# Kernel tuning notes

Measured on AMD Instinct MI355X. Metric: run time of the kernel, lower is better.

## Reference

```python
import jax, jax.numpy as jnp
import numpy as np

N_NODES = 100000
D = 128            # node feature dim == hidden_units[0]
N_EDGES = 640000
BN_EPS = 1e-3      # keras BatchNormalization default epsilon


def setup_inputs() -> dict:
    key = jax.random.key(0)
    ks = jax.random.split(key, 12)
    node_repr = jax.random.normal(ks[0], (N_NODES, D), dtype=jnp.float32)
    edges = jax.random.randint(ks[1], (2, N_EDGES), 0, N_NODES, dtype=jnp.int64)
    # ffn_prepare: BN(D) -> Dense(D, gelu)   (dropout inactive at inference)
    bn1_gamma = jax.random.normal(ks[2], (D,), dtype=jnp.float32) * 0.1 + 1.0
    bn1_beta = jax.random.normal(ks[3], (D,), dtype=jnp.float32) * 0.1
    bn1_mean = jax.random.normal(ks[4], (D,), dtype=jnp.float32) * 0.1
    bn1_var = jax.random.uniform(ks[5], (D,), dtype=jnp.float32) + 0.5
    W1 = jax.random.normal(ks[6], (D, D), dtype=jnp.float32) / np.sqrt(D)
    b1 = jnp.zeros((D,), dtype=jnp.float32)
    # update_fn: BN(2D) -> Dense(D, gelu)
    bn2_gamma = jax.random.normal(ks[7], (2 * D,), dtype=jnp.float32) * 0.1 + 1.0
    bn2_beta = jax.random.normal(ks[8], (2 * D,), dtype=jnp.float32) * 0.1
    bn2_mean = jax.random.normal(ks[9], (2 * D,), dtype=jnp.float32) * 0.1
    bn2_var = jax.random.uniform(ks[10], (2 * D,), dtype=jnp.float32) + 0.5
    W2 = jax.random.normal(ks[11], (2 * D, D), dtype=jnp.float32) / np.sqrt(2 * D)
    b2 = jnp.zeros((D,), dtype=jnp.float32)
    return dict(node_repr=node_repr, edges=edges,
                bn1_gamma=bn1_gamma, bn1_beta=bn1_beta, bn1_mean=bn1_mean, bn1_var=bn1_var,
                W1=W1, b1=b1,
                bn2_gamma=bn2_gamma, bn2_beta=bn2_beta, bn2_mean=bn2_mean, bn2_var=bn2_var,
                W2=W2, b2=b2)


def _bn(x, gamma, beta, mean, var):
    # inference-mode batch norm
    return (x - mean) * jax.lax.rsqrt(var + BN_EPS) * gamma + beta


def reference(node_repr, edges, bn1_gamma, bn1_beta, bn1_mean, bn1_var, W1, b1,
              bn2_gamma, bn2_beta, bn2_mean, bn2_var, W2, b2):
    num_nodes = node_repr.shape[0]
    node_indices, neighbour_indices = edges[0], edges[1]
    # gather neighbour features: [E, D]
    neigh = node_repr[neighbour_indices]
    # prepare FFN (BN -> dropout(identity at eval) -> Dense + exact gelu)
    msg = jax.nn.gelu(_bn(neigh, bn1_gamma, bn1_beta, bn1_mean, bn1_var) @ W1 + b1,
                      approximate=False)
    # unsorted_segment_mean: sum / count, empty segments -> 0 (TF semantics)
    sums = jax.ops.segment_sum(msg, node_indices, num_segments=num_nodes)
    cnt = jax.ops.segment_sum(jnp.ones((edges.shape[1],), msg.dtype), node_indices,
                              num_segments=num_nodes)
    agg = sums / jnp.maximum(cnt, 1.0)[:, None]
    # update FFN on concat [node_repr, agg]: [N, 2D] -> [N, D]
    h = jnp.concatenate([node_repr, agg], axis=1)
    out = jax.nn.gelu(_bn(h, bn2_gamma, bn2_beta, bn2_mean, bn2_var) @ W2 + b2,
                      approximate=False)
    return out
```

## Files before the change

kernel.cpp:

```cpp
#include <hip/hip_runtime.h>

#define NN 100000
#define DD 128
#define EE 640000
#define BN_EPS 1e-3f
#define NBLK 391
#define NTILE 6250
#define EPB 1637
#define FFN2_BLKS 768

typedef __bf16 bf16x8 __attribute__((ext_vector_type(8)));
typedef float f32x4 __attribute__((ext_vector_type(4)));

#define W1F_OFF 0u
#define W2F_OFF 32768u
#define B1F_OFF 98304u
#define B2F_OFF 98816u
#define T_OFF   99328u
#define OFFS_OFF 26099328u
#define ELIST_OFF 26899328u
#define CNTG_OFF ELIST_OFF
#define BOFS_OFF (ELIST_OFF + 611524u)
#define BSUM_OFF 29459328u
#define BOFF_OFF 29461376u
#define AGG_OFF 29464576u
#define XB_OFF  55064576u

__device__ __forceinline__ float gelu_fast(float x) {
    float x3 = x * x * x;
    float z2 = 1.5957691216057308f * x + 0.07135481627002407f * x3;
    return x / (1.0f + __expf(-z2));
}

__global__ __launch_bounds__(256) void prep_kernel(
    const float* __restrict__ g1, const float* __restrict__ be1,
    const float* __restrict__ m1, const float* __restrict__ v1,
    const float* __restrict__ W1, const float* __restrict__ b1,
    const float* __restrict__ g2, const float* __restrict__ be2,
    const float* __restrict__ m2, const float* __restrict__ v2,
    const float* __restrict__ W2, const float* __restrict__ b2,
    const int* __restrict__ edges,
    __bf16* __restrict__ W1f, __bf16* __restrict__ W2f,
    float* __restrict__ b1f, float* __restrict__ b2f,
    int* __restrict__ cntg)
{
    const int blk = blockIdx.x;
    const int t = threadIdx.x;
    if (blk < 64) {
        const int w = (blk * 256 + t) >> 6;
        const int lane = t & 63;
        if (w < 128) {
            float acc = 0.f;
            for (int k = lane; k < 128; k += 64) {
                float s = g1[k] * rsqrtf(v1[k] + BN_EPS);
                float sh = be1[k] - m1[k] * s;
                acc += sh * W1[k * 128 + w];
            }
#pragma unroll
            for (int off = 32; off > 0; off >>= 1) acc += __shfl_down(acc, off);
            if (lane == 0) b1f[w] = acc + b1[w];
        } else {
            const int n = w - 128;
            float acc = 0.f;
            for (int k = lane; k < 256; k += 64) {
                float s = g2[k] * rsqrtf(v2[k] + BN_EPS);
                float sh = be2[k] - m2[k] * s;
                acc += sh * W2[k * 128 + n];
            }
#pragma unroll
            for (int off = 32; off > 0; off >>= 1) acc += __shfl_down(acc, off);
            if (lane == 0) b2f[n] = acc + b2[n];
        }
    } else if (blk < 256) {
        int tid = (blk - 64) * 256 + t;
        if (tid < 16384) {
            int idx = tid;
            int i = idx & 7, l = (idx >> 3) & 63, nt = (idx >> 9) & 7, kt = idx >> 12;
            int k = kt * 32 + (l >> 4) * 8 + i;
            int n = nt * 16 + (l & 15);
            float s = g1[k] * rsqrtf(v1[k] + BN_EPS);
            W1f[idx] = (__bf16)(s * W1[k * 128 + n]);
        } else {
            int idx = tid - 16384;
            int i = idx & 7, l = (idx >> 3) & 63, nt = (idx >> 9) & 7, kt = idx >> 12;
            int n = nt * 16 + (l & 15);
            int row;
            if (kt < 4) {
                row = kt * 32 + (l >> 4) * 8 + i;
            } else {
                int q = (kt - 4) * 32 + (l >> 4) * 8 + i;
                row = 128 + ((q & 7) * 16 + (q >> 3));
            }
            float s = g2[row] * rsqrtf(v2[row] + BN_EPS);
            W2f[idx] = (__bf16)(s * W2[row * 128 + n]);
        }
    } else {
        __shared__ int cnt[NBLK];
        const int k = blk - 256;
        for (int b = t; b < NBLK; b += 256) cnt[b] = 0;
        __syncthreads();
        const int e0 = k * EPB, e1 = min(e0 + EPB, EE);
        for (int e = e0 + t; e < e1; e += 256)
            atomicAdd(&cnt[edges[e] >> 8], 1);
        __syncthreads();
        for (int b = t; b < NBLK; b += 256) cntg[k * NBLK + b] = cnt[b];
    }
}

__global__ __launch_bounds__(256) void sortb_kernel(const int* __restrict__ cntg,
                                                    int* __restrict__ bofs,
                                                    int* __restrict__ bsum)
{
    const int b = blockIdx.x, t = threadIdx.x;
    __shared__ int sp[256];
    int ia = 2 * t, ib = 2 * t + 1;
    int va = (ia < NBLK) ? cntg[ia * NBLK + b] : 0;
    int vb = (ib < NBLK) ? cntg[ib * NBLK + b] : 0;
    sp[t] = va + vb;
    __syncthreads();
    for (int off = 1; off < 256; off <<= 1) {
        int tmp = (t >= off) ? sp[t - off] : 0;
        __syncthreads();
        sp[t] += tmp;
        __syncthreads();
    }
    int pexcl = sp[t] - (va + vb);
    if (ia < NBLK) bofs[b * NBLK + ia] = pexcl;
    if (ib < NBLK) bofs[b * NBLK + ib] = pexcl + va;
    if (t == 255) bsum[b] = sp[255];
}

__global__ __launch_bounds__(512) void scan_top_kernel(const int* __restrict__ bsum,
                                                       int* __restrict__ boff)
{
    __shared__ int s[512];
    const int t = threadIdx.x;
    int v = (t < NBLK) ? bsum[t] : 0;
    s[t] = v;
    __syncthreads();
    for (int off = 1; off < 512; off <<= 1) {
        int tmp = (t >= off) ? s[t - off] : 0;
        __syncthreads();
        s[t] += tmp;
        __syncthreads();
    }
    if (t < NBLK) boff[t] = s[t] - v;
}

__global__ __launch_bounds__(256) void sortc_ffn1_kernel(
    const int* __restrict__ edges, const int* __restrict__ boff,
    const int* __restrict__ bofs, int* __restrict__ pairbuf,
    const float* __restrict__ X, const __bf16* __restrict__ W1f,
    const float* __restrict__ b1f, __bf16* __restrict__ T,
    __bf16* __restrict__ Xb)
{
    __shared__ __bf16 sW[16384];
    const int t = threadIdx.x;
    if (blockIdx.x < NBLK) {
        int* cur = (int*)sW;
        const int k = blockIdx.x;
        for (int b = t; b < NBLK; b += 256)
            cur[b] = boff[b] + bofs[b * NBLK + k];
        __syncthreads();
        const int e0 = k * EPB, e1 = min(e0 + EPB, EE);
        for (int e = e0 + t; e < e1; e += 256) {
            int dst = edges[e];
            int src = edges[EE + e];
            int pos = atomicAdd(&cur[dst >> 8], 1);
            pairbuf[pos] = (src << 8) | (dst & 255);
        }
        return;
    }
#pragma unroll
    for (int i = 0; i < 8; ++i) {
        int ch = i * 256 + t;
        *(bf16x8*)(sW + ch * 8) = *(const bf16x8*)(W1f + (size_t)ch * 8);
    }
    __syncthreads();

    const int wave = t >> 6;
    const int lane = t & 63;
    const int c = lane & 15, kh = lane >> 4;
    const int tbase = (blockIdx.x - NBLK) * 8;

    float bias[8];
#pragma unroll
    for (int nt = 0; nt < 8; ++nt) bias[nt] = b1f[nt * 16 + c];

#pragma unroll
    for (int s = 0; s < 2; ++s) {
        const int tile = tbase + s * 4 + wave;
        if (tile >= NTILE) break;
        const size_t rowb = (size_t)(tile * 16 + c) * DD;
        const float* xr = X + rowb + kh * 8;
        f32x4 r0[4], r1[4];
#pragma unroll
        for (int q = 0; q < 4; ++q) {
            r0[q] = *(const f32x4*)(xr + q * 32);
            r1[q] = *(const f32x4*)(xr + q * 32 + 4);
        }
        bf16x8 af[4];
#pragma unroll
        for (int kt = 0; kt < 4; ++kt) {
            bf16x8 fa;
#pragma unroll
            for (int i = 0; i < 4; ++i) { fa[i] = (__bf16)r0[kt][i]; fa[4 + i] = (__bf16)r1[kt][i]; }
            af[kt] = fa;
        }
#pragma unroll
        for (int kt = 0; kt < 4; ++kt)
            *(bf16x8*)(Xb + rowb + kt * 32 + kh * 8) = af[kt];

        f32x4 acc[8] = {};
#pragma unroll
        for (int kt = 0; kt < 4; ++kt)
#pragma unroll
            for (int nt = 0; nt < 8; ++nt) {
                bf16x8 bfr = *(const bf16x8*)(sW + ((kt * 8 + nt) * 64 + lane) * 8);
                acc[nt] = __builtin_amdgcn_mfma_f32_16x16x32_bf16(af[kt], bfr, acc[nt], 0, 0, 0);
            }
#pragma unroll
        for (int r = 0; r < 4; ++r) {
            int row = tile * 16 + kh * 4 + r;
            bf16x8 o;
#pragma unroll
            for (int nt = 0; nt < 8; ++nt)
                o[nt] = (__bf16)gelu_fast(acc[nt][r] + bias[nt]);
            *(bf16x8*)(T + (size_t)row * DD + c * 8) = o;
        }
    }
}

__global__ __launch_bounds__(256) void p2_kernel(const int* __restrict__ boff,
                                                 const int* __restrict__ pairbuf,
                                                 int* __restrict__ elist,
                                                 int* __restrict__ offs)
{
    __shared__ int s[256];
    __shared__ int cur[256];
    const int b = blockIdx.x, t = threadIdx.x;
    const int start = boff[b];
    const int end = (b + 1 < NBLK) ? boff[b + 1] : EE;
    cur[t] = 0;
    __syncthreads();
    for (int e = start + t; e < end; e += 256)
        atomicAdd(&cur[pairbuf[e] & 255], 1);
    __syncthreads();
    int v = cur[t];
    s[t] = v;
    __syncthreads();
    for (int off = 1; off < 256; off <<= 1) {
        int tmp = (t >= off) ? s[t - off] : 0;
        __syncthreads();
        s[t] += tmp;
        __syncthreads();
    }
    int ex = s[t] - v + start;
    const int node = b * 256 + t;
    if (node <= NN) offs[node] = ex;
    __syncthreads();
    cur[t] = ex;
    __syncthreads();
    for (int e = start + t; e < end; e += 256) {
        int item = pairbuf[e];
        int pos = atomicAdd(&cur[item & 255], 1);
        elist[pos] = item >> 8;
    }
}

__global__ __launch_bounds__(256) void agg_kernel(
    const __bf16* __restrict__ T, const int* __restrict__ offs,
    const int* __restrict__ elist, __bf16* __restrict__ Agg)
{
    int t = blockIdx.x * 256 + threadIdx.x;
    int node = t >> 4, j = t & 15;
    if (node >= NN) return;
    const int lane = threadIdx.x & 63;
    const int gbase = lane & 48;
    const int beg = offs[node];
    const int end = offs[node + 1];
    const int d = end - beg;
    float acc[8] = {};
    for (int eb = beg; eb < end; eb += 16) {
        int me = eb + (lane & 15);
        int sv = (me < end) ? elist[me] : 0;
        int cnt = min(end - eb, 16);
        int i = 0;
        for (; i + 3 < cnt; i += 4) {
            int s0 = __shfl(sv, gbase + i);
            int s1 = __shfl(sv, gbase + i + 1);
            int s2 = __shfl(sv, gbase + i + 2);
            int s3 = __shfl(sv, gbase + i + 3);
            bf16x8 v0 = *(const bf16x8*)(T + (size_t)s0 * DD + j * 8);
            bf16x8 v1 = *(const bf16x8*)(T + (size_t)s1 * DD + j * 8);
            bf16x8 v2 = *(const bf16x8*)(T + (size_t)s2 * DD + j * 8);
            bf16x8 v3 = *(const bf16x8*)(T + (size_t)s3 * DD + j * 8);
#pragma unroll
            for (int q = 0; q < 8; ++q)
                acc[q] += ((float)v0[q] + (float)v1[q]) + ((float)v2[q] + (float)v3[q]);
        }
        for (; i < cnt; ++i) {
            int s0 = __shfl(sv, gbase + i);
            bf16x8 v0 = *(const bf16x8*)(T + (size_t)s0 * DD + j * 8);
#pragma unroll
            for (int q = 0; q < 8; ++q) acc[q] += (float)v0[q];
        }
    }
    const float inv = 1.0f / fmaxf((float)d, 1.0f);
    bf16x8 o;
#pragma unroll
    for (int q = 0; q < 8; ++q) o[q] = (__bf16)(acc[q] * inv);
    *(bf16x8*)(Agg + (size_t)node * DD + j * 8) = o;
}

#define FFN2_LOAD(TT, XA, GA)                                              \
    {                                                                      \
        const size_t rb = (size_t)((TT) * 16 + c) * DD + kh * 8;           \
        _Pragma("unroll")                                                  \
        for (int q = 0; q < 4; ++q) {                                      \
            XA[q] = *(const bf16x8*)(Xb + rb + q * 32);                    \
            GA[q] = *(const bf16x8*)(Agg + rb + q * 32);                   \
        }                                                                  \
    }

#define FFN2_COMP(TT, XA, GA)                                              \
    {                                                                      \
        f32x4 acc0 = {}, acc1 = {};                                        \
        _Pragma("unroll")                                                  \
        for (int kt = 0; kt < 4; ++kt) {                                   \
            acc0 = __builtin_amdgcn_mfma_f32_16x16x32_bf16(XA[kt], Bf[kt][0], acc0, 0, 0, 0); \
            acc1 = __builtin_amdgcn_mfma_f32_16x16x32_bf16(XA[kt], Bf[kt][1], acc1, 0, 0, 0); \
        }                                                                  \
        _Pragma("unroll")                                                  \
        for (int kt = 0; kt < 4; ++kt) {                                   \
            acc0 = __builtin_amdgcn_mfma_f32_16x16x32_bf16(GA[kt], Bf[4 + kt][0], acc0, 0, 0, 0); \
            acc1 = __builtin_amdgcn_mfma_f32_16x16x32_bf16(GA[kt], Bf[4 + kt][1], acc1, 0, 0, 0); \
        }                                                                  \
        _Pragma("unroll")                                                  \
        for (int r = 0; r < 4; ++r) {                                      \
            int row = (TT) * 16 + kh * 4 + r;                              \
            out[(size_t)row * DD + (w * 2) * 16 + c] = gelu_fast(acc0[r] + bias0); \
            out[(size_t)row * DD + (w * 2 + 1) * 16 + c] = gelu_fast(acc1[r] + bias1); \
        }                                                                  \
    }

__global__ __launch_bounds__(256) void ffn2_kernel(
    const __bf16* __restrict__ Xb, const __bf16* __restrict__ Agg,
    const __bf16* __restrict__ W2f, const float* __restrict__ b2f,
    float* __restrict__ out)
{
    const int w = threadIdx.x >> 6;
    const int lane = threadIdx.x & 63;
    const int c = lane & 15, kh = lane >> 4;
    const int G = gridDim.x;

    bf16x8 Bf[8][2];
#pragma unroll
    for (int kt = 0; kt < 8; ++kt) {
        Bf[kt][0] = *(const bf16x8*)(W2f + ((size_t)((kt * 8 + w * 2) * 64 + lane)) * 8);
        Bf[kt][1] = *(const bf16x8*)(W2f + ((size_t)((kt * 8 + w * 2 + 1) * 64 + lane)) * 8);
    }
    const float bias0 = b2f[(w * 2) * 16 + c];
    const float bias1 = b2f[(w * 2 + 1) * 16 + c];

    int tile = blockIdx.x;
    if (tile >= NTILE) return;
    bf16x8 xa[4], ga[4], xb2[4], gb[4];
    FFN2_LOAD(tile, xa, ga);
    while (true) {
        int t2 = tile + G;
        if (t2 < NTILE) FFN2_LOAD(t2, xb2, gb);
        FFN2_COMP(tile, xa, ga);
        if (t2 >= NTILE) break;
        int t3 = t2 + G;
        if (t3 < NTILE) FFN2_LOAD(t3, xa, ga);
        FFN2_COMP(t2, xb2, gb);
        if (t3 >= NTILE) break;
        tile = t3;
    }
}

extern "C" void kernel_launch(void* const* d_in, const int* in_sizes, int n_in,
                              void* d_out, int out_size, void* d_ws, size_t ws_size,
                              hipStream_t stream) {
    const float* node_repr = (const float*)d_in[0];
    const int*   edges     = (const int*)d_in[1];
    const float* g1 = (const float*)d_in[2];
    const float* be1 = (const float*)d_in[3];
    const float* m1 = (const float*)d_in[4];
    const float* v1 = (const float*)d_in[5];
    const float* W1 = (const float*)d_in[6];
    const float* b1 = (const float*)d_in[7];
    const float* g2 = (const float*)d_in[8];
    const float* be2 = (const float*)d_in[9];
    const float* m2 = (const float*)d_in[10];
    const float* v2 = (const float*)d_in[11];
    const float* W2 = (const float*)d_in[12];
    const float* b2 = (const float*)d_in[13];

    char* ws = (char*)d_ws;
    __bf16* W1f = (__bf16*)(ws + W1F_OFF);
    __bf16* W2f = (__bf16*)(ws + W2F_OFF);
    float* b1f = (float*)(ws + B1F_OFF);
    float* b2f = (float*)(ws + B2F_OFF);
    __bf16* T  = (__bf16*)(ws + T_OFF);
    int* offs  = (int*)(ws + OFFS_OFF);
    int* elist = (int*)(ws + ELIST_OFF);
    int* cntg  = (int*)(ws + CNTG_OFF);
    int* bofs  = (int*)(ws + BOFS_OFF);
    int* bsum  = (int*)(ws + BSUM_OFF);
    int* boff  = (int*)(ws + BOFF_OFF);
    __bf16* Agg = (__bf16*)(ws + AGG_OFF);
    int* pairbuf = (int*)(ws + AGG_OFF);
    __bf16* Xb = (__bf16*)(ws + XB_OFF);
    float* out = (float*)d_out;

    hipLaunchKernelGGL(prep_kernel, dim3(256 + NBLK), dim3(256), 0, stream,
                       g1, be1, m1, v1, W1, b1, g2, be2, m2, v2, W2, b2,
                       edges, W1f, W2f, b1f, b2f, cntg);

    hipLaunchKernelGGL(sortb_kernel, dim3(NBLK), dim3(256), 0, stream, cntg, bofs, bsum);
    hipLaunchKernelGGL(scan_top_kernel, dim3(1), dim3(512), 0, stream, bsum, boff);

    hipLaunchKernelGGL(sortc_ffn1_kernel, dim3(NBLK + (NTILE + 7) / 8), dim3(256), 0, stream,
                       edges, boff, bofs, pairbuf, node_repr, W1f, b1f, T, Xb);

    hipLaunchKernelGGL(p2_kernel, dim3(NBLK), dim3(256), 0, stream,
                       boff, pairbuf, elist, offs);

    hipLaunchKernelGGL(agg_kernel, dim3((NN * 16 + 255) / 256), dim3(256), 0, stream,
                       T, offs, elist, Agg);

    hipLaunchKernelGGL(ffn2_kernel, dim3(FFN2_BLKS), dim3(256), 0, stream,
                       Xb, Agg, W2f, b2f, out);
}
```

Measured before the change: 106.7 us.

## Fold top-level scan into sort kernels and co-schedule FFN1 with bucket pass

Removes the single-block scan_top kernel. Each sortc block now recomputes the bucket prefix from bsum itself, and each p2 block computes its start offset with a wave-shuffle reduction. FFN1 tiles move out of the scatter kernel and share a launch with the per-bucket counting-sort pass, and the two tiles per wave have their global loads issued before either is computed. This cuts one launch and its serialization at the cost of redundant prefix work in every block.

```diff
diff --git a/kernel.cpp b/kernel.cpp
--- a/kernel.cpp
+++ b/kernel.cpp
@@ -7,6 +7,7 @@
 #define NBLK 391
 #define NTILE 6250
 #define EPB 1637
+#define FFN1_BLKS 782
 #define FFN2_BLKS 768
 
 typedef __bf16 bf16x8 __attribute__((ext_vector_type(8)));
@@ -22,7 +23,6 @@
 #define CNTG_OFF ELIST_OFF
 #define BOFS_OFF (ELIST_OFF + 611524u)
 #define BSUM_OFF 29459328u
-#define BOFF_OFF 29461376u
 #define AGG_OFF 29464576u
 #define XB_OFF  55064576u
 
@@ -130,26 +130,41 @@
     if (t == 255) bsum[b] = sp[255];
 }
 
-__global__ __launch_bounds__(512) void scan_top_kernel(const int* __restrict__ bsum,
-                                                       int* __restrict__ boff)
-{
-    __shared__ int s[512];
-    const int t = threadIdx.x;
-    int v = (t < NBLK) ? bsum[t] : 0;
-    s[t] = v;
+__global__ __launch_bounds__(256) void sortc_kernel(const int* __restrict__ edges,
+                                                    const int* __restrict__ bsum,
+                                                    const int* __restrict__ bofs,
+                                                    int* __restrict__ pairbuf)
+{
+    __shared__ int sp[256];
+    __shared__ int cur[NBLK];
+    const int k = blockIdx.x, t = threadIdx.x;
+    int ia = 2 * t, ib = 2 * t + 1;
+    int va = (ia < NBLK) ? bsum[ia] : 0;
+    int vb = (ib < NBLK) ? bsum[ib] : 0;
+    sp[t] = va + vb;
     __syncthreads();
-    for (int off = 1; off < 512; off <<= 1) {
-        int tmp = (t >= off) ? s[t - off] : 0;
-        __syncthreads();
-        s[t] += tmp;
-        __syncthreads();
-    }
-    if (t < NBLK) boff[t] = s[t] - v;
-}
-
-__global__ __launch_bounds__(256) void sortc_ffn1_kernel(
-    const int* __restrict__ edges, const int* __restrict__ boff,
-    const int* __restrict__ bofs, int* __restrict__ pairbuf,
+    for (int off = 1; off < 256; off <<= 1) {
+        int tmp = (t >= off) ? sp[t - off] : 0;
+        __syncthreads();
+        sp[t] += tmp;
+        __syncthreads();
+    }
+    int pexcl = sp[t] - (va + vb);
+    if (ia < NBLK) cur[ia] = pexcl + bofs[ia * NBLK + k];
+    if (ib < NBLK) cur[ib] = pexcl + va + bofs[ib * NBLK + k];
+    __syncthreads();
+    const int e0 = k * EPB, e1 = min(e0 + EPB, EE);
+    for (int e = e0 + t; e < e1; e += 256) {
+        int dst = edges[e];
+        int src = edges[EE + e];
+        int pos = atomicAdd(&cur[dst >> 8], 1);
+        pairbuf[pos] = (src << 8) | (dst & 255);
+    }
+}
+
+__global__ __launch_bounds__(256) void p2_ffn1_kernel(
+    const int* __restrict__ bsum, const int* __restrict__ pairbuf,
+    int* __restrict__ elist, int* __restrict__ offs,
     const float* __restrict__ X, const __bf16* __restrict__ W1f,
     const float* __restrict__ b1f, __bf16* __restrict__ T,
     __bf16* __restrict__ Xb)
@@ -157,17 +172,41 @@
     __shared__ __bf16 sW[16384];
     const int t = threadIdx.x;
     if (blockIdx.x < NBLK) {
-        int* cur = (int*)sW;
-        const int k = blockIdx.x;
-        for (int b = t; b < NBLK; b += 256)
-            cur[b] = boff[b] + bofs[b * NBLK + k];
-        __syncthreads();
-        const int e0 = k * EPB, e1 = min(e0 + EPB, EE);
-        for (int e = e0 + t; e < e1; e += 256) {
-            int dst = edges[e];
-            int src = edges[EE + e];
-            int pos = atomicAdd(&cur[dst >> 8], 1);
-            pairbuf[pos] = (src << 8) | (dst & 255);
+        int* sArr = (int*)sW;
+        int* cur  = sArr + 256;
+        int* red  = sArr + 512;
+        const int b = blockIdx.x;
+        int part = 0;
+        for (int i = t; i < b; i += 256) part += bsum[i];
+#pragma unroll
+        for (int off = 32; off > 0; off >>= 1) part += __shfl_down(part, off);
+        if ((t & 63) == 0) red[t >> 6] = part;
+        cur[t] = 0;
+        __syncthreads();
+        const int start = red[0] + red[1] + red[2] + red[3];
+        const int end = start + bsum[b];
+        for (int e = start + t; e < end; e += 256)
+            atomicAdd(&cur[pairbuf[e] & 255], 1);
+        __syncthreads();
+        int v = cur[t];
+        sArr[t] = v;
+        __syncthreads();
+        for (int off = 1; off < 256; off <<= 1) {
+            int tmp = (t >= off) ? sArr[t - off] : 0;
+            __syncthreads();
+            sArr[t] += tmp;
+            __syncthreads();
+        }
+        int ex = sArr[t] - v + start;
+        const int node = b * 256 + t;
+        if (node <= NN) offs[node] = ex;
+        __syncthreads();
+        cur[t] = ex;
+        __syncthreads();
+        for (int e = start + t; e < end; e += 256) {
+            int item = pairbuf[e];
+            int pos = atomicAdd(&cur[item & 255], 1);
+            elist[pos] = item >> 8;
         }
         return;
     }
@@ -182,35 +221,43 @@
     const int lane = t & 63;
     const int c = lane & 15, kh = lane >> 4;
     const int tbase = (blockIdx.x - NBLK) * 8;
+    const int tile0 = tbase + wave;
+    const int tile1 = tbase + 4 + wave;
 
     float bias[8];
 #pragma unroll
     for (int nt = 0; nt < 8; ++nt) bias[nt] = b1f[nt * 16 + c];
 
-#pragma unroll
-    for (int s = 0; s < 2; ++s) {
-        const int tile = tbase + s * 4 + wave;
-        if (tile >= NTILE) break;
-        const size_t rowb = (size_t)(tile * 16 + c) * DD;
-        const float* xr = X + rowb + kh * 8;
-        f32x4 r0[4], r1[4];
+    f32x4 r0[4], r1[4], s0[4], s1[4];
+    bf16x8 af[4];
+
+    if (tile0 < NTILE) {
+        const float* xr = X + (size_t)(tile0 * 16 + c) * DD + kh * 8;
 #pragma unroll
         for (int q = 0; q < 4; ++q) {
             r0[q] = *(const f32x4*)(xr + q * 32);
             r1[q] = *(const f32x4*)(xr + q * 32 + 4);
         }
-        bf16x8 af[4];
+    }
+    if (tile1 < NTILE) {
+        const float* xr = X + (size_t)(tile1 * 16 + c) * DD + kh * 8;
+#pragma unroll
+        for (int q = 0; q < 4; ++q) {
+            s0[q] = *(const f32x4*)(xr + q * 32);
+            s1[q] = *(const f32x4*)(xr + q * 32 + 4);
+        }
+    }
+
+    if (tile0 < NTILE) {
+        const size_t rowb = (size_t)(tile0 * 16 + c) * DD;
 #pragma unroll
         for (int kt = 0; kt < 4; ++kt) {
             bf16x8 fa;
 #pragma unroll
             for (int i = 0; i < 4; ++i) { fa[i] = (__bf16)r0[kt][i]; fa[4 + i] = (__bf16)r1[kt][i]; }
             af[kt] = fa;
-        }
-#pragma unroll
-        for (int kt = 0; kt < 4; ++kt)
-            *(bf16x8*)(Xb + rowb + kt * 32 + kh * 8) = af[kt];
-
+            *(bf16x8*)(Xb + rowb + kt * 32 + kh * 8) = fa;
+        }
         f32x4 acc[8] = {};
 #pragma unroll
         for (int kt = 0; kt < 4; ++kt)
@@ -221,7 +268,7 @@
             }
 #pragma unroll
         for (int r = 0; r < 4; ++r) {
-            int row = tile * 16 + kh * 4 + r;
+            int row = tile0 * 16 + kh * 4 + r;
             bf16x8 o;
 #pragma unroll
             for (int nt = 0; nt < 8; ++nt)
@@ -229,42 +276,33 @@
             *(bf16x8*)(T + (size_t)row * DD + c * 8) = o;
         }
     }
-}
-
-__global__ __launch_bounds__(256) void p2_kernel(const int* __restrict__ boff,
-                                                 const int* __restrict__ pairbuf,
-                                                 int* __restrict__ elist,
-                                                 int* __restrict__ offs)
-{
-    __shared__ int s[256];
-    __shared__ int cur[256];
-    const int b = blockIdx.x, t = threadIdx.x;
-    const int start = boff[b];
-    const int end = (b + 1 < NBLK) ? boff[b + 1] : EE;
-    cur[t] = 0;
-    __syncthreads();
-    for (int e = start + t; e < end; e += 256)
-        atomicAdd(&cur[pairbuf[e] & 255], 1);
-    __syncthreads();
-    int v = cur[t];
-    s[t] = v;
-    __syncthreads();
-    for (int off = 1; off < 256; off <<= 1) {
-        int tmp = (t >= off) ? s[t - off] : 0;
-        __syncthreads();
-        s[t] += tmp;
-        __syncthreads();
-    }
-    int ex = s[t] - v + start;
-    const int node = b * 256 + t;
-    if (node <= NN) offs[node] = ex;
-    __syncthreads();
-    cur[t] = ex;
-    __syncthreads();
-    for (int e = start + t; e < end; e += 256) {
-        int item = pairbuf[e];
-        int pos = atomicAdd(&cur[item & 255], 1);
-        elist[pos] = item >> 8;
+    if (tile1 < NTILE) {
+        const size_t rowb = (size_t)(tile1 * 16 + c) * DD;
+#pragma unroll
+        for (int kt = 0; kt < 4; ++kt) {
+            bf16x8 fa;
+#pragma unroll
+            for (int i = 0; i < 4; ++i) { fa[i] = (__bf16)s0[kt][i]; fa[4 + i] = (__bf16)s1[kt][i]; }
+            af[kt] = fa;
+            *(bf16x8*)(Xb + rowb + kt * 32 + kh * 8) = fa;
+        }
+        f32x4 acc[8] = {};
+#pragma unroll
+        for (int kt = 0; kt < 4; ++kt)
+#pragma unroll
+            for (int nt = 0; nt < 8; ++nt) {
+                bf16x8 bfr = *(const bf16x8*)(sW + ((kt * 8 + nt) * 64 + lane) * 8);
+                acc[nt] = __builtin_amdgcn_mfma_f32_16x16x32_bf16(af[kt], bfr, acc[nt], 0, 0, 0);
+            }
+#pragma unroll
+        for (int r = 0; r < 4; ++r) {
+            int row = tile1 * 16 + kh * 4 + r;
+            bf16x8 o;
+#pragma unroll
+            for (int nt = 0; nt < 8; ++nt)
+                o[nt] = (__bf16)gelu_fast(acc[nt][r] + bias[nt]);
+            *(bf16x8*)(T + (size_t)row * DD + c * 8) = o;
+        }
     }
 }
 
@@ -409,7 +447,6 @@
     int* cntg  = (int*)(ws + CNTG_OFF);
     int* bofs  = (int*)(ws + BOFS_OFF);
     int* bsum  = (int*)(ws + BSUM_OFF);
-    int* boff  = (int*)(ws + BOFF_OFF);
     __bf16* Agg = (__bf16*)(ws + AGG_OFF);
     int* pairbuf = (int*)(ws + AGG_OFF);
     __bf16* Xb = (__bf16*)(ws + XB_OFF);
@@ -420,13 +457,12 @@
                        edges, W1f, W2f, b1f, b2f, cntg);
 
     hipLaunchKernelGGL(sortb_kernel, dim3(NBLK), dim3(256), 0, stream, cntg, bofs, bsum);
-    hipLaunchKernelGGL(scan_top_kernel, dim3(1), dim3(512), 0, stream, bsum, boff);
-
-    hipLaunchKernelGGL(sortc_ffn1_kernel, dim3(NBLK + (NTILE + 7) / 8), dim3(256), 0, stream,
-                       edges, boff, bofs, pairbuf, node_repr, W1f, b1f, T, Xb);
-
-    hipLaunchKernelGGL(p2_kernel, dim3(NBLK), dim3(256), 0, stream,
-                       boff, pairbuf, elist, offs);
+
+    hipLaunchKernelGGL(sortc_kernel, dim3(NBLK), dim3(256), 0, stream,
+                       edges, bsum, bofs, pairbuf);
+
+    hipLaunchKernelGGL(p2_ffn1_kernel, dim3(NBLK + FFN1_BLKS), dim3(256), 0, stream,
+                       bsum, pairbuf, elist, offs, node_repr, W1f, b1f, T, Xb);
 
     hipLaunchKernelGGL(agg_kernel, dim3((NN * 16 + 255) / 256), dim3(256), 0, stream,
                        T, offs, elist, Agg);
```

Measured after the change: 104.5 us. 1.02x faster.
